# Optimization experiments

Measured on AMD Instinct MI355X. Metric: run time of the kernel, lower is better.

The kernel has to match this reference:

```python
import jax, jax.numpy as jnp
import numpy as np

# ParamsJR('JR') defaults, all variances 0 -> fixed constants; w_bb and lm are the fit params.
DT = 1e-4                      # step_size
VMAX, V0, R = 5.0, 6.0, 0.56   # sigmoid params
U_UB = 500.0                   # u_2ndsys_ub
G_EFF = 0.01 + 1000.0          # lb + relu(g)
C1_EFF, C2_EFF = 0.01 + 135.0, 0.01 + 135.0 * 0.8
C3_EFF, C4_EFF = 0.01 + 135.0 * 0.25, 0.01 + 135.0 * 0.25
STD_EFF = 150.0 + 100.0        # noise_std_lb + relu(std_in)
K_EFF = 0.5 + 5.0              # k_lb + relu(k)
A_EFF, a_EFF = 3.25, 1.0 + 100.0   # 0+relu(A), 1+relu(a)
B_EFF, b_EFF = 22.0, 1.0 + 50.0    # 0+relu(B), 1+relu(b)
CY0, Y0, MU = 5.0, 2.0, 0.5
CONDUCT_LB = 1.5


def _sig(x):
    return VMAX / (1.0 + jnp.exp(R * (V0 - x)))


def _sys2nd(A, a, u, x, v):
    return A * a * u - 2.0 * a * v - a * a * x


def _sat(x):  # state saturation 1000*tanh(x/1000)
    return 1000.0 * jnp.tanh(x / 1000.0)


def setup_inputs() -> dict:
    N, H, B, OUT, BUF = 200, 20, 400, 64, 500
    key = jax.random.key(0)
    ks = jax.random.split(key, 7)
    return {
        "input": jax.random.normal(ks[0], (N, H, B), jnp.float32),
        "noise_in": jax.random.normal(ks[1], (N, H, B, 3), jnp.float32),
        "noise_out": jax.random.normal(ks[2], (N, B), jnp.float32),
        "hx": jax.random.uniform(ks[3], (N, 6), jnp.float32),
        "hE": jnp.zeros((N, BUF), jnp.float32),
        "w_bb": jnp.full((N, N), 0.05, jnp.float32),  # zeros + 0.05 init
        "lm": jax.random.normal(ks[4], (OUT, N), jnp.float32),
        "sc": jax.random.uniform(ks[5], (N, N), jnp.float32),
        "dist": jax.random.randint(ks[6], (N, N), 0, 100, dtype=jnp.int32),
    }


def _forward(input, noise_in, noise_out, hx, hE, w_bb, lm, sc, delays):
    OUT = lm.shape[0]
    # connectivity normalization (done once, outside the time loop, as in torch)
    w = jnp.exp(w_bb) * sc
    wl = jnp.log1p(0.5 * (w + w.T))
    w_n = wl / jnp.linalg.norm(wl)             # (N,N)
    dg = -jnp.diag(jnp.sum(w_n, axis=1))       # (N,N) Laplacian diagonal
    # lead-field normalization: rowwise L1 (torch: sqrt(lm**2).sum(1)), then column mean-center
    lm1 = lm / jnp.abs(lm).sum(axis=1, keepdims=True)
    lm_t = lm1 - lm1.sum(axis=0, keepdims=True) / OUT

    def inner(carry, xs):
        M, E, I, Mv, Ev, Iv, hEb = carry
        u, nE = xs                                              # (N,1) each
        Ed = jnp.take_along_axis(hEb, delays, axis=1)           # delayed M buffer
        LEd = jnp.sum(w_n * Ed.T, axis=1, keepdims=True)        # (N,1)
        rM = _sig(E - I)
        rE = STD_EFF * nE + G_EFF * (LEd + dg @ E) + C2_EFF * _sig(C1_EFF * M)
        rI = C4_EFF * _sig(C3_EFF * M)
        ddM = M + DT * Mv
        ddE = E + DT * Ev
        ddI = I + DT * Iv
        ddMv = Mv + DT * _sys2nd(A_EFF, a_EFF, U_UB * jnp.tanh(rM / U_UB), M, Mv)
        ddEv = Ev + DT * _sys2nd(A_EFF, a_EFF, K_EFF * u + U_UB * jnp.tanh(rE / U_UB), E, Ev)
        ddIv = Iv + DT * _sys2nd(B_EFF, b_EFF, U_UB * jnp.tanh(rI / U_UB), I, Iv)
        M, E, I = _sat(ddM), _sat(ddE), _sat(ddI)
        Mv, Ev, Iv = _sat(ddMv), _sat(ddEv), _sat(ddIv)
        hEb = hEb.at[:, 0].set(M[:, 0])
        return (M, E, I, Mv, Ev, Iv, hEb), None

    def outer(carry, xs):
        u_tr, n_tr = xs                                         # (H,N,1) each
        carry, _ = jax.lax.scan(inner, carry, (u_tr, n_tr))
        M, E, I, Mv, Ev, Iv, hEb = carry
        hEb = jnp.concatenate([M, hEb[:, :-1]], axis=1)         # shift delay buffer per TR
        eeg = CY0 * (lm_t @ (E - I)) - Y0                       # (OUT,1)
        return (M, E, I, Mv, Ev, Iv, hEb), eeg[:, 0]

    M, E, I = hx[:, 0:1], hx[:, 1:2], hx[:, 2:3]
    Mv, Ev, Iv = hx[:, 3:4], hx[:, 4:5], hx[:, 5:6]
    u_all = jnp.transpose(input, (2, 1, 0))[..., None]          # (B,H,N,1)
    nE_all = jnp.transpose(noise_in[..., 0], (2, 1, 0))[..., None]
    carry, eeg = jax.lax.scan(outer, (M, E, I, Mv, Ev, Iv, hE), (u_all, nE_all))
    M, E, I, Mv, Ev, Iv, _ = carry
    current_state = jnp.concatenate([M, E, I, Mv, Ev, Iv], axis=1)  # (N,6)
    return eeg.T, current_state                                 # eeg_batch (OUT,B)


def reference(input, noise_in, noise_out, hx, hE, w_bb, lm, sc, dist):
    delays = (dist.astype(jnp.float32) / (CONDUCT_LB + MU)).astype(jnp.int32)
    return _forward(input, noise_in, noise_out, hx, hE, w_bb, lm, sc, delays)
```

## Files before the change

### kernel.cpp

```cpp
#include <hip/hip_runtime.h>
#include <math.h>

namespace {

constexpr int N_   = 200;
constexpr int H_   = 20;
constexpr int B_   = 400;
constexpr int OUT_ = 64;
constexpr int BUF_ = 500;
constexpr int NT_  = 1024;
constexpr int HD_  = 50;
constexpr int HS_  = 51;
constexpr int GT0  = 224;
constexpr int NG_  = 800;
constexpr int EPT  = 50;
constexpr int CAP  = 16;
constexpr int UNR  = 12;
constexpr int RW_  = 256;
constexpr int NFREE = NT_ - RW_;
constexpr int SLAB  = H_ * N_;

constexpr float L2E = 1.4426950408889634f;
constexpr float LN2 = 0.6931471805599453f;

constexpr float DT_  = 0.0001f;
constexpr float G_   = 1000.01f;
constexpr float C1_  = 135.01f;
constexpr float C2_  = 108.01f;
constexpr float C3_  = 33.76f;
constexpr float C4_  = 33.76f;
constexpr float STD_ = 250.0f;
constexpr float K_   = 5.5f;
constexpr float CY0_ = 5.0f;
constexpr float Y0_  = 2.0f;

constexpr float RL2E = 0.56f * L2E;
constexpr float V0R  = 6.0f * RL2E;
constexpr float TU_  = 2.0f * L2E / 500.0f;
constexpr float TS_  = 2.0f * L2E / 1000.0f;

constexpr float KMv = 0.9798f, KMu = 0.0328250f, KMx = 1.0201f;
constexpr float KEv = 0.9798f, KEu = 0.0328250f, KEx = 1.0201f;
constexpr float KIv = 0.9898f, KIu = 0.1122000f, KIx = 0.2601f;

__device__ __forceinline__ float fexp2(float x){ return __builtin_amdgcn_exp2f(x); }
__device__ __forceinline__ float flog2(float x){ return __builtin_amdgcn_logf(x); }
__device__ __forceinline__ float frcp (float x){ return __builtin_amdgcn_rcpf(x); }

__device__ __forceinline__ float sigf(float x){
    return 5.0f * frcp(1.0f + fexp2(fmaf(-RL2E, x, V0R)));
}
__device__ __forceinline__ float tanh500(float x){
    return 500.0f - 1000.0f * frcp(1.0f + fexp2(x * TU_));
}
__device__ __forceinline__ float satf(float x){
    return 1000.0f - 2000.0f * frcp(1.0f + fexp2(x * TS_));
}
__device__ __forceinline__ float wl_f(const float* __restrict__ wbb,
                                      const float* __restrict__ sc,
                                      int i, int j){
    float w0 = fexp2(wbb[i*N_+j]*L2E) * sc[i*N_+j];
    float w1 = fexp2(wbb[j*N_+i]*L2E) * sc[j*N_+i];
    return flog2(1.0f + 0.5f*(w0+w1)) * LN2;
}

__global__ void __launch_bounds__(NT_)
jansen_kernel(
    const float* __restrict__ input,
    const float* __restrict__ noise_in,
    const float* __restrict__ hx,
    const float* __restrict__ hEin,
    const float* __restrict__ wbb,
    const float* __restrict__ lm,
    const float* __restrict__ sc,
    const int*   __restrict__ dist,
    float* __restrict__ out,
    float2* __restrict__ tab)
{
    __shared__ float histT[N_*HS_];
    __shared__ float uslab[H_*N_];
    __shared__ float neslab[H_*N_];
    __shared__ float d0w_l[CAP*N_];
    __shared__ unsigned char d0j_l[CAP*N_];
    __shared__ float d1w_l[CAP*N_];
    __shared__ unsigned char d1j_l[CAP*N_];
    __shared__ float led_part[4*N_];
    __shared__ float mcol[2*N_];
    __shared__ float emi[N_];
    __shared__ float colmean[N_];
    __shared__ float lmrs[OUT_];
    __shared__ float red_s[NT_/64];
    __shared__ float norm_s;
    __shared__ int   rbar;

    const int t = threadIdx.x;
    const bool isr = (t < N_);
    const bool isg = (t >= GT0);
    const int  gt  = t - GT0;
    const int  grow  = gt >> 2;
    const int  gslot = gt & 3;
    const int  jbase = gslot * EPT;
    const int  tb    = gt * EPT;

    int sidx[5];
    int goff[5];

    if (t == 0) rbar = 0;
    if (t < OUT_){
        float s2 = 0.f;
        for (int j=0;j<N_;++j) s2 += fabsf(lm[t*N_+j]);
        lmrs[t] = s2;
    }
    float M=0,E=0,I=0,Mv=0,Ev=0,Iv=0, rowsum=0, ledst=0;
    int cnt0=0, cnt1=0;
    #pragma unroll
    for (int r=0;r<5;++r){ sidx[r]=0; goff[r]=0; }
    if (isg){
        #pragma unroll
        for (int r=0;r<5;++r){
            int p = r*NG_ + gt;
            int hh = p / N_, ii = p - hh*N_;
            sidx[r] = hh*N_ + ii;
            goff[r] = ii*(H_*B_) + hh*B_;
            uslab[sidx[r]]  = input[goff[r]];
            neslab[sidx[r]] = noise_in[goff[r]*3];
        }
    }
    if (isr){
        for (int k=1;k<HD_;++k) histT[t*HS_ + (HD_-k)] = hEin[t*BUF_+k];
        mcol[t] = hEin[t*BUF_];
        M=hx[t*6+0]; E=hx[t*6+1]; I=hx[t*6+2];
        Mv=hx[t*6+3]; Ev=hx[t*6+4]; Iv=hx[t*6+5];
    }
    __syncthreads();

    float ss = 0.f, rs = 0.f;
    for (int m=0;m<EPT;++m){
        float w = 0.f; int d = 2;
        int j = jbase + m;
        if (isg){
            d = dist[j*N_+grow] >> 1;
            w = wl_f(wbb, sc, grow, j);
        }
        ss = fmaf(w,w,ss); rs += w;
        if (isg){
            int dm = (d<2) ? 2 : d;
            float ws = (d>=2) ? w : 0.f;
            tab[tb+m] = make_float2(ws, __uint_as_float((unsigned)j | ((unsigned)dm<<16)));
        }
    }
    if (isr){
        float cm=0.f;
        for (int o=0;o<OUT_;++o) cm += lm[o*N_+t] * frcp(lmrs[o]);
        colmean[t] = cm * (1.0f/(float)OUT_);
    }
    #pragma unroll
    for (int o=32;o>0;o>>=1) ss += __shfl_down(ss,o,64);
    if ((t&63)==0) red_s[t>>6] = ss;
    __syncthreads();
    if (t==0){ float tot=0.f; for (int w=0;w<NT_/64;++w) tot+=red_s[w]; norm_s = sqrtf(tot); }
    __syncthreads();
    const float inv = 1.0f / norm_s;
    if (isg){
        float* tf = (float*)tab;
        for (int m=0;m<EPT;++m) tf[2*(tb+m)] *= inv;
    }
    if (isg) led_part[gslot*N_+grow] = rs;

    float dw[UNR]; unsigned jpk[3];
    #pragma unroll
    for (int k=0;k<UNR;++k) dw[k] = 0.f;
    jpk[0]=jpk[1]=jpk[2]=0u;
    if (isr){
        #pragma unroll
        for (int k=0;k<UNR;++k){ d0w_l[k*N_+t]=0.f; d0j_l[k*N_+t]=0;
                                 d1w_l[k*N_+t]=0.f; d1j_l[k*N_+t]=0; }
        for (int j=0;j<N_;++j){
            int dd = dist[j*N_+t] >> 1;
            if (dd < 2){
                float w = wl_f(wbb, sc, t, j) * inv;
                if (dd==0){ if (cnt0<CAP){ d0w_l[cnt0*N_+t]=w; d0j_l[cnt0*N_+t]=(unsigned char)j; ++cnt0; } }
                else      { if (cnt1<CAP){ d1w_l[cnt1*N_+t]=w; d1j_l[cnt1*N_+t]=(unsigned char)j; ++cnt1; } }
            }
        }
        #pragma unroll
        for (int k=0;k<UNR;++k){
            dw[k] = d0w_l[k*N_+t];
            unsigned jv = d0j_l[k*N_+t];
            jpk[k>>2] |= jv << ((k&3)*8);
        }
    }
    __syncthreads();

    if (isr){
        rowsum = (led_part[t]+led_part[N_+t]+led_part[2*N_+t]+led_part[3*N_+t]) * inv;
    }
    __syncthreads();

    if (isg){
        float a0 = 0.f;
        for (int m=0;m<EPT;++m){
            float2 e = tab[tb+m];
            unsigned um = __float_as_uint(e.y);
            int c = HD_ - (int)(um>>16);
            a0 = fmaf(e.x, histT[(um&0xFFFFu)*HS_ + c], a0);
        }
        led_part[gslot*N_+grow] = a0;
    }
    __syncthreads();

    if (isr){
        float v = led_part[t]+led_part[N_+t]+led_part[2*N_+t]+led_part[3*N_+t];
        #pragma unroll
        for (int k=0;k<UNR;++k)
            v = fmaf(d1w_l[k*N_+t], histT[(int)d1j_l[k*N_+t]*HS_ + 49], v);
        for (int k=UNR;k<cnt1;++k)
            v = fmaf(d1w_l[k*N_+t], histT[(int)d1j_l[k*N_+t]*HS_ + 49], v);
        ledst = v;
    }

    const int gf = t - RW_;
    int sidxM[6], goffM[6];
    bool has6 = false;
    if (t >= RW_){
        #pragma unroll
        for (int r=0;r<6;++r){
            int p = r*NFREE + gf;
            if (p < SLAB){
                int hh = p / N_, ii = p - hh*N_;
                sidxM[r] = hh*N_ + ii;
                goffM[r] = ii*(H_*B_) + hh*B_;
            } else { sidxM[r]=0; goffM[r]=0; }
        }
        has6 = (5*NFREE + gf) < SLAB;
    }
    __syncthreads();

#define ROW_BODY(MCR, MCW, HH)                                               \
    do {                                                                     \
        float rM  = sigf(E - I);                                             \
        float uM  = tanh500(rM);                                             \
        float Mn  = satf(fmaf(DT_, Mv, M));                                  \
        float Mvn = satf(fmaf(KMv, Mv, fmaf(KMu, uM, -KMx*M)));              \
        (MCW)[t] = Mn;                                                       \
        float rI  = C4_*sigf(C3_*M);                                         \
        float uI  = tanh500(rI);                                             \
        float In  = satf(fmaf(DT_, Iv, I));                                  \
        float Ivn = satf(fmaf(KIv, Iv, fmaf(KIu, uI, -KIx*I)));              \
        float u  = uslab[(HH)*N_+t];                                         \
        float ne = neslab[(HH)*N_+t];                                        \
        float l0 = ledst, l1 = 0.f, l2 = 0.f, l3 = 0.f;                      \
        _Pragma("unroll")                                                    \
        for (int k=0;k<UNR;++k){                                             \
            int j = (jpk[k>>2] >> ((k&3)*8)) & 255;                          \
            float v = (MCR)[j];                                              \
            if      ((k&3)==0) l0 = fmaf(dw[k], v, l0);                      \
            else if ((k&3)==1) l1 = fmaf(dw[k], v, l1);                      \
            else if ((k&3)==2) l2 = fmaf(dw[k], v, l2);                      \
            else               l3 = fmaf(dw[k], v, l3);                      \
        }                                                                    \
        for (int k=UNR;k<cnt0;++k)                                           \
            l0 = fmaf(d0w_l[k*N_+t], (MCR)[d0j_l[k*N_+t]], l0);              \
        float LEd = (l0+l1)+(l2+l3);                                         \
        float rE  = fmaf(STD_, ne, G_*(LEd - rowsum*E)) + C2_*sigf(C1_*M);   \
        float uE  = fmaf(K_, u, tanh500(rE));                                \
        float En  = satf(fmaf(DT_, Ev, E));                                  \
        float Evn = satf(fmaf(KEv, Ev, fmaf(KEu, uE, -KEx*E)));              \
        M=Mn; Mv=Mvn; I=In; Iv=Ivn; E=En; Ev=Evn;                            \
    } while(0)

#define ROW_SYNC()                                                           \
    do {                                                                     \
        asm volatile("s_waitcnt lgkmcnt(0)" ::: "memory");                   \
        if ((t & 63) == 0) atomicAdd(&rbar, 1);                              \
        ++repoch;                                                            \
        while (*(volatile int*)&rbar < 4*repoch)                             \
            __builtin_amdgcn_s_sleep(1);                                     \
        asm volatile("" ::: "memory");                                       \
    } while(0)

    int smod = 0;
    int repoch = 0;
    float su_r[6], sn_r[6];
    for (int s=0; s<B_; ++s){
        int ts = smod+1; if (ts==HD_) ts = 0;
        if (t < RW_){
            int cur = 0;
            #pragma unroll 2
            for (int h=0; h<H_; ++h){
                if (isr) ROW_BODY(mcol + cur*N_, mcol + (cur^1)*N_, h);
                ROW_SYNC();
                cur ^= 1;
            }
            if (isr){ histT[t*HS_ + smod] = M; emi[t] = E - I; }
        } else {
            float acc = 0.f;
            {
                const float4* t4 = (const float4*)(tab + (size_t)gf*EPT);
                #pragma unroll 5
                for (int m=0;m<EPT/2;++m){
                    float4 ee = t4[m];
                    unsigned um0 = __float_as_uint(ee.y);
                    int c0 = ts - (int)(um0>>16); if (c0<0) c0 += HD_;
                    acc = fmaf(ee.x, histT[(um0&0xFFFFu)*HS_ + c0], acc);
                    unsigned um1 = __float_as_uint(ee.w);
                    int c1 = ts - (int)(um1>>16); if (c1<0) c1 += HD_;
                    acc = fmaf(ee.z, histT[(um1&0xFFFFu)*HS_ + c1], acc);
                }
            }
            led_part[(gf&3)*N_ + (gf>>2)] = acc;
            if (gf < NG_-NFREE){
                const int u1 = NFREE + gf;
                float acc1 = 0.f;
                const float4* t4 = (const float4*)(tab + (size_t)u1*EPT);
                #pragma unroll 5
                for (int m=0;m<EPT/2;++m){
                    float4 ee = t4[m];
                    unsigned um0 = __float_as_uint(ee.y);
                    int c0 = ts - (int)(um0>>16); if (c0<0) c0 += HD_;
                    acc1 = fmaf(ee.x, histT[(um0&0xFFFFu)*HS_ + c0], acc1);
                    unsigned um1 = __float_as_uint(ee.w);
                    int c1 = ts - (int)(um1>>16); if (c1<0) c1 += HD_;
                    acc1 = fmaf(ee.z, histT[(um1&0xFFFFu)*HS_ + c1], acc1);
                }
                led_part[(u1&3)*N_ + (u1>>2)] = acc1;
            }
            int sn = s+1; if (sn >= B_) sn = B_-1;
            #pragma unroll
            for (int r=0;r<5;++r){
                su_r[r] = input[goffM[r] + sn];
                sn_r[r] = noise_in[(goffM[r] + sn)*3];
            }
            if (has6){
                su_r[5] = input[goffM[5] + sn];
                sn_r[5] = noise_in[(goffM[5] + sn)*3];
            }
        }
        __syncthreads();
        if (isr){
            float v = led_part[t]+led_part[N_+t]+led_part[2*N_+t]+led_part[3*N_+t];
            #pragma unroll
            for (int k=0;k<UNR;++k)
                v = fmaf(d1w_l[k*N_+t], mcol[d1j_l[k*N_+t]], v);
            for (int k=UNR;k<cnt1;++k)
                v = fmaf(d1w_l[k*N_+t], mcol[d1j_l[k*N_+t]], v);
            ledst = v;
        }
        if (t >= RW_){
            #pragma unroll
            for (int r=0;r<5;++r){
                uslab[sidxM[r]]  = su_r[r];
                neslab[sidxM[r]] = sn_r[r];
            }
            if (has6){ uslab[sidxM[5]] = su_r[5]; neslab[sidxM[5]] = sn_r[5]; }
        }
        {
            int o = t>>4, l = t&15;
            float il = frcp(lmrs[o]);
            float a2 = 0.f;
            for (int j=l;j<N_;j+=16)
                a2 = fmaf(fmaf(lm[o*N_+j], il, -colmean[j]), emi[j], a2);
            a2 += __shfl_down(a2,8,16); a2 += __shfl_down(a2,4,16);
            a2 += __shfl_down(a2,2,16); a2 += __shfl_down(a2,1,16);
            if (l==0) out[o*B_+s] = fmaf(CY0_, a2, -Y0_);
        }
        smod = ts;
        __syncthreads();
    }

#undef ROW_BODY
#undef ROW_SYNC

    if (isr){
        float* cs = out + OUT_*B_ + t*6;
        cs[0]=M; cs[1]=E; cs[2]=I; cs[3]=Mv; cs[4]=Ev; cs[5]=Iv;
    }
}

}

extern "C" void kernel_launch(void* const* d_in, const int* in_sizes, int n_in,
                              void* d_out, int out_size, void* d_ws, size_t ws_size,
                              hipStream_t stream)
{
    const float* input    = (const float*)d_in[0];
    const float* noise_in = (const float*)d_in[1];
    const float* hx   = (const float*)d_in[3];
    const float* hEin = (const float*)d_in[4];
    const float* wbb  = (const float*)d_in[5];
    const float* lm   = (const float*)d_in[6];
    const float* sc   = (const float*)d_in[7];
    const int*   dist = (const int*)d_in[8];
    float* out = (float*)d_out;
    float2* tab = (float2*)((char*)d_ws + 1024);

    hipLaunchKernelGGL(jansen_kernel, dim3(1), dim3(NT_), 0, stream,
                       input, noise_in, hx, hEin, wbb, lm, sc, dist, out, tab);
}
```

Before: 5.937 ms.

## Split E and M/I row updates across separate wave groups in serial loop

The per-step serial integration is split so threads 0-199 update only the E/Ev state (including the delayed-input gather), while a second group at threads 256-455 updates M, Mv, I, Iv, exchanging values through double-buffered shared arrays. The row barrier now counts eight waves instead of four, and fewer free threads remain for the history gather and input prefetch (each does more slab loads). The aim is to shorten the critical path of each inner step by running the sigmoid/tanh chains for M/I concurrently with the E chain. In exchange the spin barrier covers more waves and the background work gets fewer threads.

```diff
diff --git a/kernel.cpp b/kernel.cpp
--- a/kernel.cpp
+++ b/kernel.cpp
@@ -16,8 +16,9 @@
 constexpr int EPT  = 50;
 constexpr int CAP  = 16;
 constexpr int UNR  = 12;
-constexpr int RW_  = 256;
-constexpr int NFREE = NT_ - RW_;
+constexpr int RT_  = 512;
+constexpr int MI0  = 256;
+constexpr int NFREE = NT_ - RT_;
 constexpr int SLAB  = H_ * N_;
 
 constexpr float L2E = 1.4426950408889634f;
@@ -86,6 +87,9 @@
     __shared__ unsigned char d1j_l[CAP*N_];
     __shared__ float led_part[4*N_];
     __shared__ float mcol[2*N_];
+    __shared__ float mown[2*N_];
+    __shared__ float ecol[2*N_];
+    __shared__ float icol[N_];
     __shared__ float emi[N_];
     __shared__ float colmean[N_];
     __shared__ float lmrs[OUT_];
@@ -95,6 +99,8 @@
 
     const int t = threadIdx.x;
     const bool isr = (t < N_);
+    const bool ismi = (t >= MI0 && t < MI0+N_);
+    const int  rmi = t - MI0;
     const bool isg = (t >= GT0);
     const int  gt  = t - GT0;
     const int  grow  = gt >> 2;
@@ -129,8 +135,13 @@
     if (isr){
         for (int k=1;k<HD_;++k) histT[t*HS_ + (HD_-k)] = hEin[t*BUF_+k];
         mcol[t] = hEin[t*BUF_];
-        M=hx[t*6+0]; E=hx[t*6+1]; I=hx[t*6+2];
-        Mv=hx[t*6+3]; Ev=hx[t*6+4]; Iv=hx[t*6+5];
+        E  = hx[t*6+1];  Ev = hx[t*6+4];
+        ecol[t] = E;
+    }
+    if (ismi){
+        M  = hx[rmi*6+0]; I  = hx[rmi*6+2];
+        Mv = hx[rmi*6+3]; Iv = hx[rmi*6+5];
+        mown[rmi] = M;
     }
     __syncthreads();
 
@@ -219,12 +230,12 @@
         ledst = v;
     }
 
-    const int gf = t - RW_;
-    int sidxM[6], goffM[6];
-    bool has6 = false;
-    if (t >= RW_){
+    const int gf = t - RT_;
+    int sidxM[8], goffM[8];
+    bool has8 = false;
+    if (t >= RT_){
         #pragma unroll
-        for (int r=0;r<6;++r){
+        for (int r=0;r<8;++r){
             int p = r*NFREE + gf;
             if (p < SLAB){
                 int hh = p / N_, ii = p - hh*N_;
@@ -232,67 +243,73 @@
                 goffM[r] = ii*(H_*B_) + hh*B_;
             } else { sidxM[r]=0; goffM[r]=0; }
         }
-        has6 = (5*NFREE + gf) < SLAB;
-    }
-    __syncthreads();
-
-#define ROW_BODY(MCR, MCW, HH)                                               \
-    do {                                                                     \
-        float rM  = sigf(E - I);                                             \
-        float uM  = tanh500(rM);                                             \
-        float Mn  = satf(fmaf(DT_, Mv, M));                                  \
-        float Mvn = satf(fmaf(KMv, Mv, fmaf(KMu, uM, -KMx*M)));              \
-        (MCW)[t] = Mn;                                                       \
-        float rI  = C4_*sigf(C3_*M);                                         \
-        float uI  = tanh500(rI);                                             \
-        float In  = satf(fmaf(DT_, Iv, I));                                  \
-        float Ivn = satf(fmaf(KIv, Iv, fmaf(KIu, uI, -KIx*I)));              \
-        float u  = uslab[(HH)*N_+t];                                         \
-        float ne = neslab[(HH)*N_+t];                                        \
-        float l0 = ledst, l1 = 0.f, l2 = 0.f, l3 = 0.f;                      \
-        _Pragma("unroll")                                                    \
-        for (int k=0;k<UNR;++k){                                             \
-            int j = (jpk[k>>2] >> ((k&3)*8)) & 255;                          \
-            float v = (MCR)[j];                                              \
-            if      ((k&3)==0) l0 = fmaf(dw[k], v, l0);                      \
-            else if ((k&3)==1) l1 = fmaf(dw[k], v, l1);                      \
-            else if ((k&3)==2) l2 = fmaf(dw[k], v, l2);                      \
-            else               l3 = fmaf(dw[k], v, l3);                      \
-        }                                                                    \
-        for (int k=UNR;k<cnt0;++k)                                           \
-            l0 = fmaf(d0w_l[k*N_+t], (MCR)[d0j_l[k*N_+t]], l0);              \
-        float LEd = (l0+l1)+(l2+l3);                                         \
-        float rE  = fmaf(STD_, ne, G_*(LEd - rowsum*E)) + C2_*sigf(C1_*M);   \
-        float uE  = fmaf(K_, u, tanh500(rE));                                \
-        float En  = satf(fmaf(DT_, Ev, E));                                  \
-        float Evn = satf(fmaf(KEv, Ev, fmaf(KEu, uE, -KEx*E)));              \
-        M=Mn; Mv=Mvn; I=In; Iv=Ivn; E=En; Ev=Evn;                            \
-    } while(0)
+        has8 = (7*NFREE + gf) < SLAB;
+    }
+    __syncthreads();
 
 #define ROW_SYNC()                                                           \
     do {                                                                     \
         asm volatile("s_waitcnt lgkmcnt(0)" ::: "memory");                   \
         if ((t & 63) == 0) atomicAdd(&rbar, 1);                              \
         ++repoch;                                                            \
-        while (*(volatile int*)&rbar < 4*repoch)                             \
+        while (*(volatile int*)&rbar < 8*repoch)                             \
             __builtin_amdgcn_s_sleep(1);                                     \
         asm volatile("" ::: "memory");                                       \
     } while(0)
 
     int smod = 0;
     int repoch = 0;
-    float su_r[6], sn_r[6];
+    float su_r[8], sn_r[8];
     for (int s=0; s<B_; ++s){
         int ts = smod+1; if (ts==HD_) ts = 0;
-        if (t < RW_){
+        if (t < RT_){
             int cur = 0;
             #pragma unroll 2
             for (int h=0; h<H_; ++h){
-                if (isr) ROW_BODY(mcol + cur*N_, mcol + (cur^1)*N_, h);
+                if (isr){
+                    float Mh = mown[cur*N_+t];
+                    float u  = uslab[h*N_+t];
+                    float ne = neslab[h*N_+t];
+                    const float* MCR = mcol + cur*N_;
+                    float l0 = ledst, l1 = 0.f, l2 = 0.f, l3 = 0.f;
+                    #pragma unroll
+                    for (int k=0;k<UNR;++k){
+                        int j = (jpk[k>>2] >> ((k&3)*8)) & 255;
+                        float v = MCR[j];
+                        if      ((k&3)==0) l0 = fmaf(dw[k], v, l0);
+                        else if ((k&3)==1) l1 = fmaf(dw[k], v, l1);
+                        else if ((k&3)==2) l2 = fmaf(dw[k], v, l2);
+                        else               l3 = fmaf(dw[k], v, l3);
+                    }
+                    for (int k=UNR;k<cnt0;++k)
+                        l0 = fmaf(d0w_l[k*N_+t], MCR[d0j_l[k*N_+t]], l0);
+                    float LEd = (l0+l1)+(l2+l3);
+                    float rE  = fmaf(STD_, ne, G_*(LEd - rowsum*E)) + C2_*sigf(C1_*Mh);
+                    float uE  = fmaf(K_, u, tanh500(rE));
+                    float En  = satf(fmaf(DT_, Ev, E));
+                    float Evn = satf(fmaf(KEv, Ev, fmaf(KEu, uE, -KEx*E)));
+                    ecol[(cur^1)*N_+t] = En;
+                    E = En; Ev = Evn;
+                } else if (ismi){
+                    float Eh  = ecol[cur*N_+rmi];
+                    float rM  = sigf(Eh - I);
+                    float uM  = tanh500(rM);
+                    float Mn  = satf(fmaf(DT_, Mv, M));
+                    float Mvn = satf(fmaf(KMv, Mv, fmaf(KMu, uM, -KMx*M)));
+                    mcol[(cur^1)*N_+rmi] = Mn;
+                    mown[(cur^1)*N_+rmi] = Mn;
+                    float rI  = C4_*sigf(C3_*M);
+                    float uI  = tanh500(rI);
+                    float In  = satf(fmaf(DT_, Iv, I));
+                    float Ivn = satf(fmaf(KIv, Iv, fmaf(KIu, uI, -KIx*I)));
+                    icol[rmi] = In;
+                    M=Mn; Mv=Mvn; I=In; Iv=Ivn;
+                }
                 ROW_SYNC();
                 cur ^= 1;
             }
-            if (isr){ histT[t*HS_ + smod] = M; emi[t] = E - I; }
+            if (ismi) histT[rmi*HS_ + smod] = M;
+            if (isr)  emi[t] = E - icol[t];
         } else {
             float acc = 0.f;
             {
@@ -327,13 +344,13 @@
             }
             int sn = s+1; if (sn >= B_) sn = B_-1;
             #pragma unroll
-            for (int r=0;r<5;++r){
+            for (int r=0;r<7;++r){
                 su_r[r] = input[goffM[r] + sn];
                 sn_r[r] = noise_in[(goffM[r] + sn)*3];
             }
-            if (has6){
-                su_r[5] = input[goffM[5] + sn];
-                sn_r[5] = noise_in[(goffM[5] + sn)*3];
+            if (has8){
+                su_r[7] = input[goffM[7] + sn];
+                sn_r[7] = noise_in[(goffM[7] + sn)*3];
             }
         }
         __syncthreads();
@@ -346,13 +363,13 @@
                 v = fmaf(d1w_l[k*N_+t], mcol[d1j_l[k*N_+t]], v);
             ledst = v;
         }
-        if (t >= RW_){
+        if (t >= RT_){
             #pragma unroll
-            for (int r=0;r<5;++r){
+            for (int r=0;r<7;++r){
                 uslab[sidxM[r]]  = su_r[r];
                 neslab[sidxM[r]] = sn_r[r];
             }
-            if (has6){ uslab[sidxM[5]] = su_r[5]; neslab[sidxM[5]] = sn_r[5]; }
+            if (has8){ uslab[sidxM[7]] = su_r[7]; neslab[sidxM[7]] = sn_r[7]; }
         }
         {
             int o = t>>4, l = t&15;
@@ -368,12 +385,15 @@
         __syncthreads();
     }
 
-#undef ROW_BODY
 #undef ROW_SYNC
 
     if (isr){
         float* cs = out + OUT_*B_ + t*6;
-        cs[0]=M; cs[1]=E; cs[2]=I; cs[3]=Mv; cs[4]=Ev; cs[5]=Iv;
+        cs[1]=E; cs[4]=Ev;
+    }
+    if (ismi){
+        float* cs = out + OUT_*B_ + rmi*6;
+        cs[0]=M; cs[2]=I; cs[3]=Mv; cs[5]=Iv;
     }
 }
 
```

Result: slower. 7.065 ms (+19.0%).

## Advance two inner steps per barrier using precomputed M pairs

Applied to the files above, without the earlier changes.

The intra-TR recurrence is restructured so each round of the short-delay coupling reads a pair (M at step h, M at step h+1) from a double-buffered float2 array. Because M_{h+1} depends only on M_h and Mv_h, two integration steps can be computed per round. This halves the number of spin barriers among the 256 row threads per TR, from 20 to 10. The cost is more register pressure, duplicated gather FMAs and a change in when M values are published, which risks subtle ordering errors (for example, the d1 gather now reads the .x slot).

```diff
diff --git a/kernel.cpp b/kernel.cpp
--- a/kernel.cpp
+++ b/kernel.cpp
@@ -85,7 +85,7 @@
     __shared__ float d1w_l[CAP*N_];
     __shared__ unsigned char d1j_l[CAP*N_];
     __shared__ float led_part[4*N_];
-    __shared__ float mcol[2*N_];
+    __shared__ float2 mpair[2*N_];
     __shared__ float emi[N_];
     __shared__ float colmean[N_];
     __shared__ float lmrs[OUT_];
@@ -111,7 +111,7 @@
         for (int j=0;j<N_;++j) s2 += fabsf(lm[t*N_+j]);
         lmrs[t] = s2;
     }
-    float M=0,E=0,I=0,Mv=0,Ev=0,Iv=0, rowsum=0, ledst=0;
+    float M=0,E=0,I=0,Mv=0,Ev=0,Iv=0, rowsum=0, ledst=0, hE0v=0;
     int cnt0=0, cnt1=0;
     #pragma unroll
     for (int r=0;r<5;++r){ sidx[r]=0; goff[r]=0; }
@@ -128,7 +128,7 @@
     }
     if (isr){
         for (int k=1;k<HD_;++k) histT[t*HS_ + (HD_-k)] = hEin[t*BUF_+k];
-        mcol[t] = hEin[t*BUF_];
+        hE0v = hEin[t*BUF_];
         M=hx[t*6+0]; E=hx[t*6+1]; I=hx[t*6+2];
         Mv=hx[t*6+3]; Ev=hx[t*6+4]; Iv=hx[t*6+5];
     }
@@ -234,40 +234,13 @@
         }
         has6 = (5*NFREE + gf) < SLAB;
     }
-    __syncthreads();
-
-#define ROW_BODY(MCR, MCW, HH)                                               \
-    do {                                                                     \
-        float rM  = sigf(E - I);                                             \
-        float uM  = tanh500(rM);                                             \
-        float Mn  = satf(fmaf(DT_, Mv, M));                                  \
-        float Mvn = satf(fmaf(KMv, Mv, fmaf(KMu, uM, -KMx*M)));              \
-        (MCW)[t] = Mn;                                                       \
-        float rI  = C4_*sigf(C3_*M);                                         \
-        float uI  = tanh500(rI);                                             \
-        float In  = satf(fmaf(DT_, Iv, I));                                  \
-        float Ivn = satf(fmaf(KIv, Iv, fmaf(KIu, uI, -KIx*I)));              \
-        float u  = uslab[(HH)*N_+t];                                         \
-        float ne = neslab[(HH)*N_+t];                                        \
-        float l0 = ledst, l1 = 0.f, l2 = 0.f, l3 = 0.f;                      \
-        _Pragma("unroll")                                                    \
-        for (int k=0;k<UNR;++k){                                             \
-            int j = (jpk[k>>2] >> ((k&3)*8)) & 255;                          \
-            float v = (MCR)[j];                                              \
-            if      ((k&3)==0) l0 = fmaf(dw[k], v, l0);                      \
-            else if ((k&3)==1) l1 = fmaf(dw[k], v, l1);                      \
-            else if ((k&3)==2) l2 = fmaf(dw[k], v, l2);                      \
-            else               l3 = fmaf(dw[k], v, l3);                      \
-        }                                                                    \
-        for (int k=UNR;k<cnt0;++k)                                           \
-            l0 = fmaf(d0w_l[k*N_+t], (MCR)[d0j_l[k*N_+t]], l0);              \
-        float LEd = (l0+l1)+(l2+l3);                                         \
-        float rE  = fmaf(STD_, ne, G_*(LEd - rowsum*E)) + C2_*sigf(C1_*M);   \
-        float uE  = fmaf(K_, u, tanh500(rE));                                \
-        float En  = satf(fmaf(DT_, Ev, E));                                  \
-        float Evn = satf(fmaf(KEv, Ev, fmaf(KEu, uE, -KEx*E)));              \
-        M=Mn; Mv=Mvn; I=In; Iv=Ivn; E=En; Ev=Evn;                            \
-    } while(0)
+
+    float M1r = 0.f;
+    if (isr){
+        M1r = satf(fmaf(DT_, Mv, M));
+        mpair[t] = make_float2(hE0v, M1r);
+    }
+    __syncthreads();
 
 #define ROW_SYNC()                                                           \
     do {                                                                     \
@@ -285,12 +258,61 @@
     for (int s=0; s<B_; ++s){
         int ts = smod+1; if (ts==HD_) ts = 0;
         if (t < RW_){
-            int cur = 0;
-            #pragma unroll 2
-            for (int h=0; h<H_; ++h){
-                if (isr) ROW_BODY(mcol + cur*N_, mcol + (cur^1)*N_, h);
-                ROW_SYNC();
-                cur ^= 1;
+            #pragma unroll 1
+            for (int kb=0; kb<10; ++kb){
+                if (isr){
+                    const float2* rb = mpair + (kb&1)*N_;
+                    float2*       wb = mpair + ((kb+1)&1)*N_;
+                    float g0=ledst, g1=0.f, g2=0.f, g3=0.f;
+                    float f0=ledst, f1=0.f, f2=0.f, f3=0.f;
+                    #pragma unroll
+                    for (int k=0;k<UNR;++k){
+                        int j = (jpk[k>>2] >> ((k&3)*8)) & 255;
+                        float2 mj = rb[j];
+                        float w = dw[k];
+                        if      ((k&3)==0){ g0=fmaf(w,mj.x,g0); f0=fmaf(w,mj.y,f0); }
+                        else if ((k&3)==1){ g1=fmaf(w,mj.x,g1); f1=fmaf(w,mj.y,f1); }
+                        else if ((k&3)==2){ g2=fmaf(w,mj.x,g2); f2=fmaf(w,mj.y,f2); }
+                        else              { g3=fmaf(w,mj.x,g3); f3=fmaf(w,mj.y,f3); }
+                    }
+                    for (int k=UNR;k<cnt0;++k){
+                        float w = d0w_l[k*N_+t];
+                        float2 mj = rb[d0j_l[k*N_+t]];
+                        g0=fmaf(w,mj.x,g0); f0=fmaf(w,mj.y,f0);
+                    }
+                    float LEd0 = (g0+g1)+(g2+g3);
+                    float LEd1 = (f0+f1)+(f2+f3);
+                    float E1s = satf(fmaf(DT_, Ev, E));
+                    float I1s = satf(fmaf(DT_, Iv, I));
+                    float uM0 = tanh500(sigf(E - I));
+                    float Mv1 = satf(fmaf(KMv, Mv, fmaf(KMu, uM0, -KMx*M)));
+                    float M2  = satf(fmaf(DT_, Mv1, M1r));
+                    float uM1 = tanh500(sigf(E1s - I1s));
+                    float Mv2 = satf(fmaf(KMv, Mv1, fmaf(KMu, uM1, -KMx*M1r)));
+                    float M3  = satf(fmaf(DT_, Mv2, M2));
+                    wb[t] = make_float2(M2, M3);
+                    float uI0 = tanh500(C4_*sigf(C3_*M));
+                    float Iv1 = satf(fmaf(KIv, Iv, fmaf(KIu, uI0, -KIx*I)));
+                    float I2  = satf(fmaf(DT_, Iv1, I1s));
+                    float uI1 = tanh500(C4_*sigf(C3_*M1r));
+                    float Iv2 = satf(fmaf(KIv, Iv1, fmaf(KIu, uI1, -KIx*I1s)));
+                    int h0 = 2*kb;
+                    float u0  = uslab[h0*N_+t];
+                    float ne0 = neslab[h0*N_+t];
+                    float rE0 = fmaf(STD_, ne0, G_*(LEd0 - rowsum*E)) + C2_*sigf(C1_*M);
+                    float uE0 = fmaf(K_, u0, tanh500(rE0));
+                    float Ev1 = satf(fmaf(KEv, Ev, fmaf(KEu, uE0, -KEx*E)));
+                    float E2  = satf(fmaf(DT_, Ev1, E1s));
+                    float u1  = uslab[(h0+1)*N_+t];
+                    float ne1 = neslab[(h0+1)*N_+t];
+                    float rE1 = fmaf(STD_, ne1, G_*(LEd1 - rowsum*E1s)) + C2_*sigf(C1_*M1r);
+                    float uE1 = fmaf(K_, u1, tanh500(rE1));
+                    float Ev2 = satf(fmaf(KEv, Ev1, fmaf(KEu, uE1, -KEx*E1s)));
+                    M=M2; M1r=M3; Mv=Mv2;
+                    I=I2; Iv=Iv2;
+                    E=E2; Ev=Ev2;
+                }
+                if (kb < 9) ROW_SYNC();
             }
             if (isr){ histT[t*HS_ + smod] = M; emi[t] = E - I; }
         } else {
@@ -341,9 +363,9 @@
             float v = led_part[t]+led_part[N_+t]+led_part[2*N_+t]+led_part[3*N_+t];
             #pragma unroll
             for (int k=0;k<UNR;++k)
-                v = fmaf(d1w_l[k*N_+t], mcol[d1j_l[k*N_+t]], v);
+                v = fmaf(d1w_l[k*N_+t], mpair[d0j_l[0]*0 + d1j_l[k*N_+t]].x, v);
             for (int k=UNR;k<cnt1;++k)
-                v = fmaf(d1w_l[k*N_+t], mcol[d1j_l[k*N_+t]], v);
+                v = fmaf(d1w_l[k*N_+t], mpair[d1j_l[k*N_+t]].x, v);
             ledst = v;
         }
         if (t >= RW_){
@@ -368,7 +390,6 @@
         __syncthreads();
     }
 
-#undef ROW_BODY
 #undef ROW_SYNC
 
     if (isr){
```

After: 5.923 ms. Within noise of the previous version (-0.2%).

## Spread 200 row threads across 8 waves with 25 lanes each

Applied to the files above, without the earlier changes.

The row-update threads are remapped so each of 8 wavefronts handles 25 rows, instead of 4 fully packed waves. The aim is to spread the serial per-row recurrence across more SIMDs and cut per-wave latency in the inner H loop. In exchange, the custom inter-wave barrier now waits on 8 waves, and fewer threads remain for the delayed-coupling and slab-prefetch work, so each free thread loads 8 slab entries instead of 6.

```diff
diff --git a/kernel.cpp b/kernel.cpp
--- a/kernel.cpp
+++ b/kernel.cpp
@@ -16,8 +16,9 @@
 constexpr int EPT  = 50;
 constexpr int CAP  = 16;
 constexpr int UNR  = 12;
-constexpr int RW_  = 256;
-constexpr int NFREE = NT_ - RW_;
+constexpr int RT_  = 512;
+constexpr int RPW  = 25;
+constexpr int NFREE = NT_ - RT_;
 constexpr int SLAB  = H_ * N_;
 
 constexpr float L2E = 1.4426950408889634f;
@@ -94,6 +95,10 @@
     __shared__ int   rbar;
 
     const int t = threadIdx.x;
+    const int lane = t & 63;
+    const int wv   = t >> 6;
+    const bool isrow = (t < RT_) && (lane < RPW);
+    const int  r     = wv*RPW + lane;
     const bool isr = (t < N_);
     const bool isg = (t >= GT0);
     const int  gt  = t - GT0;
@@ -114,23 +119,25 @@
     float M=0,E=0,I=0,Mv=0,Ev=0,Iv=0, rowsum=0, ledst=0;
     int cnt0=0, cnt1=0;
     #pragma unroll
-    for (int r=0;r<5;++r){ sidx[r]=0; goff[r]=0; }
+    for (int rr=0;rr<5;++rr){ sidx[rr]=0; goff[rr]=0; }
     if (isg){
         #pragma unroll
-        for (int r=0;r<5;++r){
-            int p = r*NG_ + gt;
+        for (int rr=0;rr<5;++rr){
+            int p = rr*NG_ + gt;
             int hh = p / N_, ii = p - hh*N_;
-            sidx[r] = hh*N_ + ii;
-            goff[r] = ii*(H_*B_) + hh*B_;
-            uslab[sidx[r]]  = input[goff[r]];
-            neslab[sidx[r]] = noise_in[goff[r]*3];
+            sidx[rr] = hh*N_ + ii;
+            goff[rr] = ii*(H_*B_) + hh*B_;
+            uslab[sidx[rr]]  = input[goff[rr]];
+            neslab[sidx[rr]] = noise_in[goff[rr]*3];
         }
     }
     if (isr){
         for (int k=1;k<HD_;++k) histT[t*HS_ + (HD_-k)] = hEin[t*BUF_+k];
         mcol[t] = hEin[t*BUF_];
-        M=hx[t*6+0]; E=hx[t*6+1]; I=hx[t*6+2];
-        Mv=hx[t*6+3]; Ev=hx[t*6+4]; Iv=hx[t*6+5];
+    }
+    if (isrow){
+        M=hx[r*6+0]; E=hx[r*6+1]; I=hx[r*6+2];
+        Mv=hx[r*6+3]; Ev=hx[r*6+4]; Iv=hx[r*6+5];
     }
     __syncthreads();
 
@@ -171,29 +178,29 @@
     #pragma unroll
     for (int k=0;k<UNR;++k) dw[k] = 0.f;
     jpk[0]=jpk[1]=jpk[2]=0u;
-    if (isr){
+    if (isrow){
         #pragma unroll
-        for (int k=0;k<UNR;++k){ d0w_l[k*N_+t]=0.f; d0j_l[k*N_+t]=0;
-                                 d1w_l[k*N_+t]=0.f; d1j_l[k*N_+t]=0; }
+        for (int k=0;k<UNR;++k){ d0w_l[k*N_+r]=0.f; d0j_l[k*N_+r]=0;
+                                 d1w_l[k*N_+r]=0.f; d1j_l[k*N_+r]=0; }
         for (int j=0;j<N_;++j){
-            int dd = dist[j*N_+t] >> 1;
+            int dd = dist[j*N_+r] >> 1;
             if (dd < 2){
-                float w = wl_f(wbb, sc, t, j) * inv;
-                if (dd==0){ if (cnt0<CAP){ d0w_l[cnt0*N_+t]=w; d0j_l[cnt0*N_+t]=(unsigned char)j; ++cnt0; } }
-                else      { if (cnt1<CAP){ d1w_l[cnt1*N_+t]=w; d1j_l[cnt1*N_+t]=(unsigned char)j; ++cnt1; } }
+                float w = wl_f(wbb, sc, r, j) * inv;
+                if (dd==0){ if (cnt0<CAP){ d0w_l[cnt0*N_+r]=w; d0j_l[cnt0*N_+r]=(unsigned char)j; ++cnt0; } }
+                else      { if (cnt1<CAP){ d1w_l[cnt1*N_+r]=w; d1j_l[cnt1*N_+r]=(unsigned char)j; ++cnt1; } }
             }
         }
         #pragma unroll
         for (int k=0;k<UNR;++k){
-            dw[k] = d0w_l[k*N_+t];
-            unsigned jv = d0j_l[k*N_+t];
+            dw[k] = d0w_l[k*N_+r];
+            unsigned jv = d0j_l[k*N_+r];
             jpk[k>>2] |= jv << ((k&3)*8);
         }
     }
     __syncthreads();
 
-    if (isr){
-        rowsum = (led_part[t]+led_part[N_+t]+led_part[2*N_+t]+led_part[3*N_+t]) * inv;
+    if (isrow){
+        rowsum = (led_part[r]+led_part[N_+r]+led_part[2*N_+r]+led_part[3*N_+r]) * inv;
     }
     __syncthreads();
 
@@ -209,30 +216,30 @@
     }
     __syncthreads();
 
-    if (isr){
-        float v = led_part[t]+led_part[N_+t]+led_part[2*N_+t]+led_part[3*N_+t];
+    if (isrow){
+        float v = led_part[r]+led_part[N_+r]+led_part[2*N_+r]+led_part[3*N_+r];
         #pragma unroll
         for (int k=0;k<UNR;++k)
-            v = fmaf(d1w_l[k*N_+t], histT[(int)d1j_l[k*N_+t]*HS_ + 49], v);
+            v = fmaf(d1w_l[k*N_+r], histT[(int)d1j_l[k*N_+r]*HS_ + 49], v);
         for (int k=UNR;k<cnt1;++k)
-            v = fmaf(d1w_l[k*N_+t], histT[(int)d1j_l[k*N_+t]*HS_ + 49], v);
+            v = fmaf(d1w_l[k*N_+r], histT[(int)d1j_l[k*N_+r]*HS_ + 49], v);
         ledst = v;
     }
 
-    const int gf = t - RW_;
-    int sidxM[6], goffM[6];
-    bool has6 = false;
-    if (t >= RW_){
+    const int gf = t - RT_;
+    int sidxM[8], goffM[8];
+    bool has8 = false;
+    if (t >= RT_){
         #pragma unroll
-        for (int r=0;r<6;++r){
-            int p = r*NFREE + gf;
+        for (int rr=0;rr<8;++rr){
+            int p = rr*NFREE + gf;
             if (p < SLAB){
                 int hh = p / N_, ii = p - hh*N_;
-                sidxM[r] = hh*N_ + ii;
-                goffM[r] = ii*(H_*B_) + hh*B_;
-            } else { sidxM[r]=0; goffM[r]=0; }
-        }
-        has6 = (5*NFREE + gf) < SLAB;
+                sidxM[rr] = hh*N_ + ii;
+                goffM[rr] = ii*(H_*B_) + hh*B_;
+            } else { sidxM[rr]=0; goffM[rr]=0; }
+        }
+        has8 = (7*NFREE + gf) < SLAB;
     }
     __syncthreads();
 
@@ -242,13 +249,13 @@
         float uM  = tanh500(rM);                                             \
         float Mn  = satf(fmaf(DT_, Mv, M));                                  \
         float Mvn = satf(fmaf(KMv, Mv, fmaf(KMu, uM, -KMx*M)));              \
-        (MCW)[t] = Mn;                                                       \
+        (MCW)[r] = Mn;                                                       \
         float rI  = C4_*sigf(C3_*M);                                         \
         float uI  = tanh500(rI);                                             \
         float In  = satf(fmaf(DT_, Iv, I));                                  \
         float Ivn = satf(fmaf(KIv, Iv, fmaf(KIu, uI, -KIx*I)));              \
-        float u  = uslab[(HH)*N_+t];                                         \
-        float ne = neslab[(HH)*N_+t];                                        \
+        float u  = uslab[(HH)*N_+r];                                         \
+        float ne = neslab[(HH)*N_+r];                                        \
         float l0 = ledst, l1 = 0.f, l2 = 0.f, l3 = 0.f;                      \
         _Pragma("unroll")                                                    \
         for (int k=0;k<UNR;++k){                                             \
@@ -260,7 +267,7 @@
             else               l3 = fmaf(dw[k], v, l3);                      \
         }                                                                    \
         for (int k=UNR;k<cnt0;++k)                                           \
-            l0 = fmaf(d0w_l[k*N_+t], (MCR)[d0j_l[k*N_+t]], l0);              \
+            l0 = fmaf(d0w_l[k*N_+r], (MCR)[d0j_l[k*N_+r]], l0);              \
         float LEd = (l0+l1)+(l2+l3);                                         \
         float rE  = fmaf(STD_, ne, G_*(LEd - rowsum*E)) + C2_*sigf(C1_*M);   \
         float uE  = fmaf(K_, u, tanh500(rE));                                \
@@ -274,25 +281,25 @@
         asm volatile("s_waitcnt lgkmcnt(0)" ::: "memory");                   \
         if ((t & 63) == 0) atomicAdd(&rbar, 1);                              \
         ++repoch;                                                            \
-        while (*(volatile int*)&rbar < 4*repoch)                             \
+        while (*(volatile int*)&rbar < 8*repoch)                             \
             __builtin_amdgcn_s_sleep(1);                                     \
         asm volatile("" ::: "memory");                                       \
     } while(0)
 
     int smod = 0;
     int repoch = 0;
-    float su_r[6], sn_r[6];
+    float su_r[8], sn_r[8];
     for (int s=0; s<B_; ++s){
         int ts = smod+1; if (ts==HD_) ts = 0;
-        if (t < RW_){
+        if (t < RT_){
             int cur = 0;
             #pragma unroll 2
             for (int h=0; h<H_; ++h){
-                if (isr) ROW_BODY(mcol + cur*N_, mcol + (cur^1)*N_, h);
+                if (isrow) ROW_BODY(mcol + cur*N_, mcol + (cur^1)*N_, h);
                 ROW_SYNC();
                 cur ^= 1;
             }
-            if (isr){ histT[t*HS_ + smod] = M; emi[t] = E - I; }
+            if (isrow){ histT[r*HS_ + smod] = M; emi[r] = E - I; }
         } else {
             float acc = 0.f;
             {
@@ -327,32 +334,32 @@
             }
             int sn = s+1; if (sn >= B_) sn = B_-1;
             #pragma unroll
-            for (int r=0;r<5;++r){
-                su_r[r] = input[goffM[r] + sn];
-                sn_r[r] = noise_in[(goffM[r] + sn)*3];
-            }
-            if (has6){
-                su_r[5] = input[goffM[5] + sn];
-                sn_r[5] = noise_in[(goffM[5] + sn)*3];
+            for (int rr=0;rr<7;++rr){
+                su_r[rr] = input[goffM[rr] + sn];
+                sn_r[rr] = noise_in[(goffM[rr] + sn)*3];
+            }
+            if (has8){
+                su_r[7] = input[goffM[7] + sn];
+                sn_r[7] = noise_in[(goffM[7] + sn)*3];
             }
         }
         __syncthreads();
-        if (isr){
-            float v = led_part[t]+led_part[N_+t]+led_part[2*N_+t]+led_part[3*N_+t];
+        if (isrow){
+            float v = led_part[r]+led_part[N_+r]+led_part[2*N_+r]+led_part[3*N_+r];
             #pragma unroll
             for (int k=0;k<UNR;++k)
-                v = fmaf(d1w_l[k*N_+t], mcol[d1j_l[k*N_+t]], v);
+                v = fmaf(d1w_l[k*N_+r], mcol[d1j_l[k*N_+r]], v);
             for (int k=UNR;k<cnt1;++k)
-                v = fmaf(d1w_l[k*N_+t], mcol[d1j_l[k*N_+t]], v);
+                v = fmaf(d1w_l[k*N_+r], mcol[d1j_l[k*N_+r]], v);
             ledst = v;
         }
-        if (t >= RW_){
+        if (t >= RT_){
             #pragma unroll
-            for (int r=0;r<5;++r){
-                uslab[sidxM[r]]  = su_r[r];
-                neslab[sidxM[r]] = sn_r[r];
-            }
-            if (has6){ uslab[sidxM[5]] = su_r[5]; neslab[sidxM[5]] = sn_r[5]; }
+            for (int rr=0;rr<7;++rr){
+                uslab[sidxM[rr]]  = su_r[rr];
+                neslab[sidxM[rr]] = sn_r[rr];
+            }
+            if (has8){ uslab[sidxM[7]] = su_r[7]; neslab[sidxM[7]] = sn_r[7]; }
         }
         {
             int o = t>>4, l = t&15;
@@ -371,8 +378,8 @@
 #undef ROW_BODY
 #undef ROW_SYNC
 
-    if (isr){
-        float* cs = out + OUT_*B_ + t*6;
+    if (isrow){
+        float* cs = out + OUT_*B_ + r*6;
         cs[0]=M; cs[1]=E; cs[2]=I; cs[3]=Mv; cs[4]=Ev; cs[5]=Iv;
     }
 }
```

New measurement: 8.228 ms. 38.6% more time.
